# Optimization experiments

Hardware: AMD Instinct MI355X
Metric: run time of the kernel (lower is better)

The kernel has to match this reference:

```python
import jax, jax.numpy as jnp
import numpy as np
jax.config.update("jax_enable_x64", True)  # hash math needs int64 like torch .long()

NUM_LEVELS = 16
BASE_RES = 16
LOG2_HASHMAP = 19
FEAT_DIM = 2
N_POINTS = 2097152
PRIMES = (1, 2654435761, 805459861)


def setup_inputs() -> dict:
    key = jax.random.key(0)
    k1, k2 = jax.random.split(key)
    xyz = jax.random.uniform(k1, (N_POINTS, 3), dtype=jnp.float32)
    # 16 hash tables of shape [2**19, 2], init randn * 0.1 as in the module
    tables = jax.random.normal(
        k2, (NUM_LEVELS, 2 ** LOG2_HASHMAP, FEAT_DIM), dtype=jnp.float32) * 0.1
    return {"xyz": xyz, "tables": tables}


def reference(xyz, tables):
    L, F = NUM_LEVELS, FEAT_DIM
    N = xyz.shape[0]
    grid_res = (BASE_RES * (2 ** jnp.arange(L, dtype=jnp.int64)))  # [L]
    # scale + truncate-to-int per level (xyz >= 0 so trunc == floor, matches .long())
    scaled = xyz[None, :, :] * grid_res[:, None, None].astype(xyz.dtype)  # [L, N, 3]
    idx = scaled.astype(jnp.int64)  # [L, N, 3]
    # spatial hash: (x*1) ^ (y*p1) ^ (z*p2) mod 2**19
    h = (idx[..., 0] * PRIMES[0]) ^ (idx[..., 1] * PRIMES[1]) ^ (idx[..., 2] * PRIMES[2])
    h = h % (1 << LOG2_HASHMAP)  # [L, N], non-negative
    # per-level gather from its own table
    feats = jax.vmap(lambda t, hh: t[hh])(tables, h)  # [L, N, F]
    # concat level features along last dim -> [N, L*F]
    return jnp.transpose(feats, (1, 0, 2)).reshape(N, L * F)
```

## Files before the change

kernel.cpp:

```cpp
#include <hip/hip_runtime.h>

#define NUM_LEVELS 16
#define LOG2_HASHMAP 19
#define TABLE_SIZE (1u << LOG2_HASHMAP)
#define PPT 8

typedef unsigned long long u64;

__global__ __launch_bounds__(256) void gather_kernel(
    const float* __restrict__ xyz,
    const float* __restrict__ tables,
    u64* __restrict__ ws,
    int n_points, int blocks_per_level, int stride_pts)
{
    int b     = blockIdx.x;
    int xcd   = b & 7;
    int j     = b >> 3;
    int phase = (j >= blocks_per_level) ? 1 : 0;
    int l     = xcd + (phase << 3);
    int jj    = j - phase * blocks_per_level;
    int base  = jj * 256 + (int)threadIdx.x;

    const u64* tbl = (const u64*)tables + ((size_t)l << LOG2_HASHMAP);
    u64* wsl = ws + (size_t)l * n_points;
    int shift = 15 - l;

    unsigned hh[PPT];
    int      nn[PPT];
    bool     ok[PPT];
#pragma unroll
    for (int s = 0; s < PPT; ++s) {
        int n = base + s * stride_pts;
        nn[s] = n;
        ok[s] = (n < n_points);
        int ncl = ok[s] ? n : 0;
        float x = xyz[ncl * 3 + 0];
        float y = xyz[ncl * 3 + 1];
        float z = xyz[ncl * 3 + 2];
        unsigned wx = (unsigned)(x * 524288.0f) >> shift;
        unsigned wy = (unsigned)(y * 524288.0f) >> shift;
        unsigned wz = (unsigned)(z * 524288.0f) >> shift;
        hh[s] = (wx ^ (wy * 2654435761u) ^ (wz * 805459861u)) & (TABLE_SIZE - 1u);
    }

    u64 f[PPT];
#pragma unroll
    for (int s = 0; s < PPT; ++s)
        f[s] = tbl[hh[s]];

#pragma unroll
    for (int s = 0; s < PPT; ++s)
        if (ok[s])
            __builtin_nontemporal_store(f[s], wsl + nn[s]);
}

__global__ __launch_bounds__(256) void transpose_kernel(
    const u64* __restrict__ ws,
    u64* __restrict__ out,
    int n_points)
{
    __shared__ u64 tile[128][NUM_LEVELS + 1];
    int n0 = blockIdx.x * 128;

    for (int i = threadIdx.x; i < 128 * NUM_LEVELS; i += 256) {
        int l = i >> 7;
        int n = i & 127;
        int gn = n0 + n;
        u64 v = (gn < n_points)
                  ? __builtin_nontemporal_load(ws + (size_t)l * n_points + gn)
                  : 0ull;
        tile[n][l] = v;
    }
    __syncthreads();

    for (int i = threadIdx.x; i < 128 * NUM_LEVELS; i += 256) {
        int n = i >> 4;
        int l = i & 15;
        if (n0 + n < n_points)
            __builtin_nontemporal_store(tile[n][l], out + (size_t)n0 * NUM_LEVELS + i);
    }
}

__global__ __launch_bounds__(256) void fused_kernel(
    const float* __restrict__ xyz,
    const float* __restrict__ tables,
    u64* __restrict__ out,
    int n_points)
{
    int tid = blockIdx.x * blockDim.x + threadIdx.x;
    int n = tid >> 4;
    int l = tid & 15;
    if (n >= n_points) return;
    float x = xyz[n * 3 + 0], y = xyz[n * 3 + 1], z = xyz[n * 3 + 2];
    float res = (float)(16u << l);
    unsigned ix = (unsigned)(x * res);
    unsigned iy = (unsigned)(y * res);
    unsigned iz = (unsigned)(z * res);
    unsigned h = (ix ^ (iy * 2654435761u) ^ (iz * 805459861u)) & (TABLE_SIZE - 1u);
    u64 f = *((const u64*)tables + (((size_t)l << LOG2_HASHMAP) + h));
    out[(size_t)n * NUM_LEVELS + l] = f;
}

extern "C" void kernel_launch(void* const* d_in, const int* in_sizes, int n_in,
                              void* d_out, int out_size, void* d_ws, size_t ws_size,
                              hipStream_t stream) {
    const float* xyz    = (const float*)d_in[0];
    const float* tables = (const float*)d_in[1];

    int n_points = in_sizes[0] / 3;
    size_t ws_needed = (size_t)n_points * NUM_LEVELS * sizeof(u64);

    if (ws_size >= ws_needed) {
        int blocks_per_level = (n_points + 256 * PPT - 1) / (256 * PPT);
        int stride_pts = blocks_per_level * 256;
        int grid1 = blocks_per_level * NUM_LEVELS;
        gather_kernel<<<grid1, 256, 0, stream>>>(
            xyz, tables, (u64*)d_ws, n_points, blocks_per_level, stride_pts);

        int grid2 = (n_points + 127) / 128;
        transpose_kernel<<<grid2, 256, 0, stream>>>(
            (const u64*)d_ws, (u64*)d_out, n_points);
    } else {
        int total = n_points * NUM_LEVELS;
        int grid = (total + 255) / 256;
        fused_kernel<<<grid, 256, 0, stream>>>(xyz, tables, (u64*)d_out, n_points);
    }
}
```

Measured before the change: 319.3 us.

## Pre-pack quantized coordinates into u64 and vectorize transpose kernel accesses

Adds a pack kernel that quantizes each point's xyz once into a single 64-bit word, so the 16 per-level gather passes each read 8 bytes per point instead of 12 bytes from three scattered float loads. This needs extra workspace and one more launch. The transpose kernel is also reworked to read and write 16-byte vector chunks, with the shared tile laid out level-major and padded. If the workspace is too small, the code falls back to the original xyz-based gather.

```diff
diff --git a/kernel.cpp b/kernel.cpp
--- a/kernel.cpp
+++ b/kernel.cpp
@@ -6,8 +6,67 @@
 #define PPT 8
 
 typedef unsigned long long u64;
-
-__global__ __launch_bounds__(256) void gather_kernel(
+typedef unsigned long long u64x2 __attribute__((ext_vector_type(2)));
+
+__global__ __launch_bounds__(256) void pack_kernel(
+    const float* __restrict__ xyz, u64* __restrict__ w, int n_points)
+{
+    int n = blockIdx.x * 256 + threadIdx.x;
+    if (n >= n_points) return;
+    float x = xyz[n * 3 + 0];
+    float y = xyz[n * 3 + 1];
+    float z = xyz[n * 3 + 2];
+    u64 wx = (unsigned)(x * 524288.0f);
+    u64 wy = (unsigned)(y * 524288.0f);
+    u64 wz = (unsigned)(z * 524288.0f);
+    w[n] = wx | (wy << 19) | (wz << 38);
+}
+
+__global__ __launch_bounds__(256) void gather_kernel_w(
+    const u64* __restrict__ w,
+    const float* __restrict__ tables,
+    u64* __restrict__ ws,
+    int n_points, int blocks_per_level, int stride_pts)
+{
+    int b     = blockIdx.x;
+    int xcd   = b & 7;
+    int j     = b >> 3;
+    int phase = (j >= blocks_per_level) ? 1 : 0;
+    int l     = xcd + (phase << 3);
+    int jj    = j - phase * blocks_per_level;
+    int base  = jj * 256 + (int)threadIdx.x;
+
+    const u64* tbl = (const u64*)tables + ((size_t)l << LOG2_HASHMAP);
+    u64* wsl = ws + (size_t)l * n_points;
+    int shift = 15 - l;
+
+    unsigned hh[PPT];
+    int      nn[PPT];
+    bool     ok[PPT];
+#pragma unroll
+    for (int s = 0; s < PPT; ++s) {
+        int n = base + s * stride_pts;
+        nn[s] = n;
+        ok[s] = (n < n_points);
+        u64 wp = __builtin_nontemporal_load(w + (ok[s] ? n : 0));
+        unsigned wx = (unsigned)(wp & 0x7FFFFu) >> shift;
+        unsigned wy = (unsigned)((wp >> 19) & 0x7FFFFu) >> shift;
+        unsigned wz = (unsigned)((wp >> 38) & 0x7FFFFu) >> shift;
+        hh[s] = (wx ^ (wy * 2654435761u) ^ (wz * 805459861u)) & (TABLE_SIZE - 1u);
+    }
+
+    u64 f[PPT];
+#pragma unroll
+    for (int s = 0; s < PPT; ++s)
+        f[s] = tbl[hh[s]];
+
+#pragma unroll
+    for (int s = 0; s < PPT; ++s)
+        if (ok[s])
+            __builtin_nontemporal_store(f[s], wsl + nn[s]);
+}
+
+__global__ __launch_bounds__(256) void gather_kernel_xyz(
     const float* __restrict__ xyz,
     const float* __restrict__ tables,
     u64* __restrict__ ws,
@@ -42,16 +101,12 @@
         unsigned wz = (unsigned)(z * 524288.0f) >> shift;
         hh[s] = (wx ^ (wy * 2654435761u) ^ (wz * 805459861u)) & (TABLE_SIZE - 1u);
     }
-
     u64 f[PPT];
 #pragma unroll
+    for (int s = 0; s < PPT; ++s) f[s] = tbl[hh[s]];
+#pragma unroll
     for (int s = 0; s < PPT; ++s)
-        f[s] = tbl[hh[s]];
-
-#pragma unroll
-    for (int s = 0; s < PPT; ++s)
-        if (ok[s])
-            __builtin_nontemporal_store(f[s], wsl + nn[s]);
+        if (ok[s]) __builtin_nontemporal_store(f[s], wsl + nn[s]);
 }
 
 __global__ __launch_bounds__(256) void transpose_kernel(
@@ -59,25 +114,36 @@
     u64* __restrict__ out,
     int n_points)
 {
-    __shared__ u64 tile[128][NUM_LEVELS + 1];
+    __shared__ u64 tile[NUM_LEVELS][129];
     int n0 = blockIdx.x * 128;
 
-    for (int i = threadIdx.x; i < 128 * NUM_LEVELS; i += 256) {
-        int l = i >> 7;
-        int n = i & 127;
-        int gn = n0 + n;
-        u64 v = (gn < n_points)
-                  ? __builtin_nontemporal_load(ws + (size_t)l * n_points + gn)
-                  : 0ull;
-        tile[n][l] = v;
+    for (int i = threadIdx.x; i < 64 * NUM_LEVELS; i += 256) {
+        int l  = i >> 6;
+        int np = (i & 63) << 1;
+        int gn = n0 + np;
+        u64 a = 0, bb = 0;
+        if (gn + 1 < n_points) {
+            u64x2 v = __builtin_nontemporal_load(
+                (const u64x2*)(ws + (size_t)l * n_points + gn));
+            a = v.x; bb = v.y;
+        } else if (gn < n_points) {
+            a = __builtin_nontemporal_load(ws + (size_t)l * n_points + gn);
+        }
+        tile[l][np]     = a;
+        tile[l][np + 1] = bb;
     }
     __syncthreads();
 
-    for (int i = threadIdx.x; i < 128 * NUM_LEVELS; i += 256) {
-        int n = i >> 4;
-        int l = i & 15;
-        if (n0 + n < n_points)
-            __builtin_nontemporal_store(tile[n][l], out + (size_t)n0 * NUM_LEVELS + i);
+    for (int i = threadIdx.x; i < 128 * (NUM_LEVELS / 2); i += 256) {
+        int n  = i >> 3;
+        int lp = i & 7;
+        if (n0 + n < n_points) {
+            u64x2 v;
+            v.x = tile[2 * lp][n];
+            v.y = tile[2 * lp + 1][n];
+            __builtin_nontemporal_store(
+                v, (u64x2*)(out + ((size_t)(n0 + n) * NUM_LEVELS + 2 * lp)));
+        }
     }
 }
 
@@ -108,14 +174,23 @@
     const float* tables = (const float*)d_in[1];
 
     int n_points = in_sizes[0] / 3;
-    size_t ws_needed = (size_t)n_points * NUM_LEVELS * sizeof(u64);
-
-    if (ws_size >= ws_needed) {
+    size_t ws_main = (size_t)n_points * NUM_LEVELS * sizeof(u64);
+    size_t ws_pack = ws_main + (size_t)n_points * sizeof(u64);
+
+    if (ws_size >= ws_main) {
         int blocks_per_level = (n_points + 256 * PPT - 1) / (256 * PPT);
         int stride_pts = blocks_per_level * 256;
         int grid1 = blocks_per_level * NUM_LEVELS;
-        gather_kernel<<<grid1, 256, 0, stream>>>(
-            xyz, tables, (u64*)d_ws, n_points, blocks_per_level, stride_pts);
+
+        if (ws_size >= ws_pack) {
+            u64* w = (u64*)d_ws + (size_t)n_points * NUM_LEVELS;
+            pack_kernel<<<(n_points + 255) / 256, 256, 0, stream>>>(xyz, w, n_points);
+            gather_kernel_w<<<grid1, 256, 0, stream>>>(
+                w, tables, (u64*)d_ws, n_points, blocks_per_level, stride_pts);
+        } else {
+            gather_kernel_xyz<<<grid1, 256, 0, stream>>>(
+                xyz, tables, (u64*)d_ws, n_points, blocks_per_level, stride_pts);
+        }
 
         int grid2 = (n_points + 127) / 128;
         transpose_kernel<<<grid2, 256, 0, stream>>>(
```

Result: slower. 370.5 us (+16.0%).
